# Performance work log

Hardware: AMD Instinct MI355X
Metric: run time of the kernel (lower is better)

Reference implementation:

```python
import jax, jax.numpy as jnp
import numpy as np

B, T, D, SPAN = 4, 4096, 1024, 128


def _windowed_attention(q, k, v, span):
    # Causal sliding-window attention: position t attends to [max(0, t-span+1), t].
    # Tiled as blocks of size span: each query block attends to its own block
    # plus the previous block (exactly covers the window), avoiding any [T,T]
    # or per-timestep materialization.
    B, T, D = q.shape
    S = span
    nb = T // S  # T chosen divisible by span
    qb = q.reshape(B, nb, S, D)
    kb = k.reshape(B, nb, S, D)
    vb = v.reshape(B, nb, S, D)
    pad = jnp.zeros((B, 1, S, D), dtype=q.dtype)
    kk = jnp.concatenate([jnp.concatenate([pad, kb[:, :-1]], axis=1), kb], axis=2)  # [B,nb,2S,D]
    vv = jnp.concatenate([jnp.concatenate([pad, vb[:, :-1]], axis=1), vb], axis=2)  # [B,nb,2S,D]
    scale = 1.0 / jnp.sqrt(jnp.asarray(D, dtype=q.dtype))
    scores = jnp.einsum('bnqd,bnkd->bnqk', qb, kk) * scale  # [B,nb,S,2S]
    n_idx = jnp.arange(nb)[:, None, None]      # block index
    q_idx = jnp.arange(S)[None, :, None]       # query offset within block
    k_idx = jnp.arange(2 * S)[None, None, :]   # key offset in [prev|cur] pair
    rel = k_idx - S - q_idx                    # key_pos - query_pos
    # window: -span+1 <= rel <= 0; first block's "previous" half is padding -> mask it
    mask = (rel <= 0) & (rel > -S) & ((n_idx > 0) | (k_idx >= S))
    neg = jnp.asarray(jnp.finfo(scores.dtype).min, dtype=scores.dtype)
    scores = jnp.where(mask, scores, neg)
    w = jax.nn.softmax(scores, axis=-1)
    out = jnp.einsum('bnqk,bnkd->bnqd', w, vv)
    return out.reshape(B, T, D)


def setup_inputs() -> dict:
    key = jax.random.key(0)
    ks = jax.random.split(key, 7)
    s = 1.0 / np.sqrt(D)
    return {
        'x': jax.random.normal(ks[0], (B, T, D), dtype=jnp.float32),
        'Wq': jax.random.normal(ks[1], (D, D), dtype=jnp.float32) * s,
        'bq': jax.random.normal(ks[2], (D,), dtype=jnp.float32) * s,
        'Wk': jax.random.normal(ks[3], (D, D), dtype=jnp.float32) * s,
        'bk': jax.random.normal(ks[4], (D,), dtype=jnp.float32) * s,
        'Wv': jax.random.normal(ks[5], (D, D), dtype=jnp.float32) * s,
        'bv': jax.random.normal(ks[6], (D,), dtype=jnp.float32) * s,
        'span': SPAN,
    }


def reference(x, Wq, bq, Wk, bk, Wv, bv, span):
    # torch nn.Linear: y = x @ W.T + b
    q = jnp.einsum('btd,ed->bte', x, Wq) + bq
    k = jnp.einsum('btd,ed->bte', x, Wk) + bk
    v = jnp.einsum('btd,ed->bte', x, Wv) + bv
    return _windowed_attention(q, k, v, span)
```

## Files before the change

kernel.cpp:

```cpp
#include <hip/hip_runtime.h>
#include <hip/hip_bf16.h>

#define BB 4
#define TT 4096
#define DD 1024
#define SS 128
#define MM (BB*TT)

typedef __attribute__((ext_vector_type(8))) short bf16x8;
typedef __attribute__((ext_vector_type(4))) short s16x4;
typedef __attribute__((ext_vector_type(4))) float f32x4;

#define VMCNT(N) asm volatile("s_waitcnt vmcnt(" #N ")" ::: "memory")
#define LGKM0()  asm volatile("s_waitcnt lgkmcnt(0)" ::: "memory")

__device__ __forceinline__ void block_sync() {
    asm volatile("" ::: "memory");
    __builtin_amdgcn_s_barrier();
    asm volatile("" ::: "memory");
}

__device__ __forceinline__ short f2bf(float f) {
    union { float f; unsigned u; } cv; cv.f = f;
    unsigned u = cv.u;
    u += 0x7fffu + ((u >> 16) & 1u);
    return (short)(u >> 16);
}

__device__ __forceinline__ void gload16(const short* g, short* l) {
    __builtin_amdgcn_global_load_lds(
        (const __attribute__((address_space(1))) void*)g,
        (__attribute__((address_space(3))) void*)l, 16, 0, 0);
}

__global__ __launch_bounds__(256) void cast_f32_bf16(
    const float* __restrict__ src, short* __restrict__ dst)
{
    const int i = (blockIdx.x * 256 + threadIdx.x) * 4;
    const float4 v = *(const float4*)(src + i);
    s16x4 o;
    o.x = f2bf(v.x); o.y = f2bf(v.y); o.z = f2bf(v.z); o.w = f2bf(v.w);
    *(s16x4*)(dst + i) = o;
}

__global__ __launch_bounds__(256) void cast_w3(
    const float* __restrict__ a, const float* __restrict__ b,
    const float* __restrict__ c, short* __restrict__ dst)
{
    const float* src = (blockIdx.y == 0) ? a : (blockIdx.y == 1) ? b : c;
    short* d = dst + (size_t)blockIdx.y * DD * DD;
    const int i = (blockIdx.x * 256 + threadIdx.x) * 4;
    const float4 v = *(const float4*)(src + i);
    s16x4 o;
    o.x = f2bf(v.x); o.y = f2bf(v.y); o.z = f2bf(v.z); o.w = f2bf(v.w);
    *(s16x4*)(d + i) = o;
}


#define MF(a_, b_, c_) ((GRP == 2)                                            \
    ? __builtin_amdgcn_mfma_f32_16x16x32_bf16((b_), (a_), (c_), 0, 0, 0)      \
    : __builtin_amdgcn_mfma_f32_16x16x32_bf16((a_), (b_), (c_), 0, 0, 0))

#define QKV_PHASE(ABASE, P, STAGE_STMT, VM_STMT)                              \
  do {                                                                        \
    bf16x8 af0k0 = *(const bf16x8*)((ABASE) + (((P)*2)*16   + c16) * 64 + sw0);\
    bf16x8 af0k1 = *(const bf16x8*)((ABASE) + (((P)*2)*16   + c16) * 64 + sw1);\
    bf16x8 af1k0 = *(const bf16x8*)((ABASE) + (((P)*2+1)*16 + c16) * 64 + sw0);\
    bf16x8 af1k1 = *(const bf16x8*)((ABASE) + (((P)*2+1)*16 + c16) * 64 + sw1);\
    STAGE_STMT;                                                               \
    block_sync();                                                             \
    LGKM0();                                                                  \
    __builtin_amdgcn_s_setprio(1);                                            \
    _Pragma("unroll")                                                         \
    for (int nj = 0; nj < 4; nj++) {                                          \
      acc[(P)*2][nj]   = MF(af0k0, bf[nj][0], acc[(P)*2][nj]);                \
      acc[(P)*2][nj]   = MF(af0k1, bf[nj][1], acc[(P)*2][nj]);                \
      acc[(P)*2+1][nj] = MF(af1k0, bf[nj][0], acc[(P)*2+1][nj]);              \
      acc[(P)*2+1][nj] = MF(af1k1, bf[nj][1], acc[(P)*2+1][nj]);              \
    }                                                                         \
    __builtin_amdgcn_s_setprio(0);                                            \
    VM_STMT;                                                                  \
    block_sync();                                                             \
  } while (0)

template<int GRP>
__device__ __forceinline__ void qkv_core(
    const short* __restrict__ X, const short* __restrict__ W,
    const float* __restrict__ bias,
    short* __restrict__ Y, short* __restrict__ vT,
    short* lds, const int m_base, const int n_base)
{
    const int tid  = threadIdx.x;
    const int wv   = tid >> 6, lane = tid & 63;
    const int wm   = wv >> 2,  wn   = wv & 3;
    const int quad = lane >> 4, c16 = lane & 15;
    const int swz  = c16 & 7;
    const int sw0  = ((quad)     ^ swz) * 8;
    const int sw1  = ((quad + 4) ^ swz) * 8;

    auto stageA = [&](int k0, int d, int h) {
        short* dst = lds + d * 16384 + h * 8192;
#pragma unroll
        for (int g = 0; g < 2; g++) {
            const int idx = g * 512 + tid;
            const int row = idx >> 3, slot = idx & 7;
            gload16(X + (size_t)(m_base + h * 128 + row) * DD + k0
                      + ((slot ^ (row & 7)) * 8),
                    dst + row * 64 + slot * 8);
        }
    };
    auto stageB = [&](int k0, int d, int h) {
        short* dst = lds + 32768 + d * 16384 + h * 8192;
#pragma unroll
        for (int g = 0; g < 2; g++) {
            const int idx = g * 512 + tid;
            const int row = idx >> 3, slot = idx & 7;
            gload16(W + (size_t)(n_base + h * 128 + row) * DD + k0
                      + ((slot ^ (row & 7)) * 8),
                    dst + row * 64 + slot * 8);
        }
    };

    f32x4 acc[8][4];
#pragma unroll
    for (int i = 0; i < 8; i++)
#pragma unroll
        for (int j = 0; j < 4; j++) acc[i][j] = (f32x4){0.f, 0.f, 0.f, 0.f};

    stageA(0, 0, 0);  stageA(0, 0, 1);
    stageB(0, 0, 0);  stageB(0, 0, 1);
    stageB(64, 1, 0); stageB(64, 1, 1);
    VMCNT(4);
    block_sync();

    const short* Abuf0 = lds + wm * 8192;
    const short* Abuf1 = lds + 16384 + wm * 8192;
    const short* Bbuf0 = lds + 32768 + (wn >> 1) * 8192 + (wn & 1) * 4096;
    const short* Bbuf1 = lds + 49152 + (wn >> 1) * 8192 + (wn & 1) * 4096;

    bf16x8 bf[4][2];

    for (int it = 0; it < 8; ++it) {
        const int k1 = it * 128 + 64;
        const int k2 = it * 128 + 128;
        const int k3 = it * 128 + 192;
        const bool more = (it < 7);

#pragma unroll
        for (int nj = 0; nj < 4; nj++) {
            bf[nj][0] = *(const bf16x8*)(Bbuf0 + (nj * 16 + c16) * 64 + sw0);
            bf[nj][1] = *(const bf16x8*)(Bbuf0 + (nj * 16 + c16) * 64 + sw1);
        }
        QKV_PHASE(Abuf0, 0, stageA(k1, 1, 0), ((void)0));
        QKV_PHASE(Abuf0, 1, stageA(k1, 1, 1), ((void)0));
        QKV_PHASE(Abuf0, 2, if (more) stageB(k2, 0, 0), ((void)0));
        QKV_PHASE(Abuf0, 3, if (more) stageB(k2, 0, 1),
                  if (more) { VMCNT(4); } else { VMCNT(0); });

#pragma unroll
        for (int nj = 0; nj < 4; nj++) {
            bf[nj][0] = *(const bf16x8*)(Bbuf1 + (nj * 16 + c16) * 64 + sw0);
            bf[nj][1] = *(const bf16x8*)(Bbuf1 + (nj * 16 + c16) * 64 + sw1);
        }
        QKV_PHASE(Abuf1, 0, if (more) stageA(k2, 0, 0), ((void)0));
        QKV_PHASE(Abuf1, 1, if (more) stageA(k2, 0, 1), ((void)0));
        QKV_PHASE(Abuf1, 2, if (more) stageB(k3, 1, 0), ((void)0));
        QKV_PHASE(Abuf1, 3, if (more) stageB(k3, 1, 1),
                  if (more) { VMCNT(4); } else { VMCNT(0); });
    }

    if (GRP != 2) {
#pragma unroll
        for (int nj = 0; nj < 4; nj++) {
            const int col = n_base + wn * 64 + nj * 16 + c16;
            const float bc = bias[col];
#pragma unroll
            for (int mi = 0; mi < 8; mi++) {
                const int row = m_base + wm * 128 + mi * 16 + quad * 4;
#pragma unroll
                for (int r = 0; r < 4; r++)
                    Y[(size_t)(row + r) * DD + col] = f2bf(acc[mi][nj][r] + bc);
            }
        }
    } else {
#pragma unroll
        for (int nj = 0; nj < 4; nj++) {
#pragma unroll
            for (int r = 0; r < 4; r++) {
                const int drow = n_base + wn * 64 + nj * 16 + quad * 4 + r;
                const float bc = bias[drow];
#pragma unroll
                for (int mi = 0; mi < 8; mi++) {
                    const int mcol = m_base + wm * 128 + mi * 16 + c16;
                    vT[((size_t)(mcol >> 12) * DD + drow) * TT + (mcol & 4095)]
                        = f2bf(acc[mi][nj][r] + bc);
                }
            }
        }
    }
}

__global__ __launch_bounds__(512, 2) void qkv_gemm8(
    const short* __restrict__ X, const short* __restrict__ W3,
    const float* __restrict__ bq, const float* __restrict__ bk,
    const float* __restrict__ bv,
    short* __restrict__ q, short* __restrict__ k, short* __restrict__ vT)
{
    __shared__ __align__(16) short lds[65536];
    const int bid = blockIdx.x;
    const int wg  = (bid & 7) * 96 + (bid >> 3);
    const int mt  = wg & 63;
    const int cn  = wg >> 6;
    const int grp = cn >> 2;
    const int nt  = cn & 3;
    const int m_base = mt * 256;
    const int n_base = nt * 256;
    if (grp == 0)      qkv_core<0>(X, W3,              bq, q, nullptr, lds, m_base, n_base);
    else if (grp == 1) qkv_core<1>(X, W3 + DD * DD,    bk, k, nullptr, lds, m_base, n_base);
    else               qkv_core<2>(X, W3 + 2 * DD * DD, bv, nullptr, vT, lds, m_base, n_base);
}

__global__ __launch_bounds__(512, 2) void attn_fused(
    const short* __restrict__ Q,
    const short* __restrict__ Kb,
    const short* __restrict__ VT,
    float* __restrict__ O)
{
    __shared__ short lds[78336];

    const int l   = blockIdx.x;
    const int xcd = l & 7;
    const int rr  = l >> 3;
    const int n   = xcd * 4 + (rr & 3);
    const int qh  = (rr >> 2) & 1;
    const int b   = rr >> 3;

    const int tid  = threadIdx.x;
    const int wv   = tid >> 6, lane = tid & 63;
    const int quad = lane >> 4, c16 = lane & 15;
    const int qt   = wv >> 1;
    const int kh   = wv & 1;
    const int dh   = wv & 1;

    const int qrow   = b * TT + n * SS + qh * 64;
    const int krow   = b * TT + n * SS - SS;
    const int bstart = b * TT;

    f32x4 acc[8];
#pragma unroll
    for (int j = 0; j < 8; j++) acc[j] = (f32x4){0.f, 0.f, 0.f, 0.f};

    auto stage1 = [&](int kk, int bi) {
        short* qb = lds + bi * 20480;
        short* kb = qb + 4096;
        const int k0 = kk * 64;
        {
            const int row = tid >> 3, slot = tid & 7;
            gload16(Q + (qrow + row) * DD + k0 + ((slot ^ (row & 7)) * 8),
                    qb + row * 64 + slot * 8);
        }
#pragma unroll
        for (int g = 0; g < 4; g++) {
            const int idx = g * 512 + tid;
            const int row = idx >> 3, slot = idx & 7;
            int grow = krow + row;
            if (grow < bstart) grow = bstart;
            gload16(Kb + grow * DD + k0 + ((slot ^ (row & 7)) * 8),
                    kb + row * 64 + slot * 8);
        }
    };

    const int sw7 = c16 & 7;

    stage1(0, 0);
    stage1(1, 1);
    for (int kk = 0; kk < 16; kk++) {
        if (kk < 15) { VMCNT(5); } else { VMCNT(0); }
        block_sync();
        if (kk < 14) stage1(kk + 2, (kk + 2) % 3);
        const short* qb = lds + (kk % 3) * 20480;
        const short* kb = qb + 4096;
        __builtin_amdgcn_s_setprio(1);
#pragma unroll
        for (int ks = 0; ks < 2; ks++) {
            const int slot = ((ks * 4 + quad) ^ sw7) * 8;
            bf16x8 a = *(const bf16x8*)(qb + (qt * 16 + c16) * 64 + slot);
#pragma unroll
            for (int j = 0; j < 8; j++) {
                bf16x8 bf = *(const bf16x8*)(kb + (kh * 128 + j * 16 + c16) * 64 + slot);
                acc[j] = __builtin_amdgcn_mfma_f32_16x16x32_bf16(a, bf, acc[j], 0, 0, 0);
            }
        }
        __builtin_amdgcn_s_setprio(0);
    }

    block_sync();

    const int tbase = n * SS - SS;
    auto stage2 = [&](int s, int bi) {
        short* vb = lds + bi * 16384;
        const int d0  = (s >> 1) * 128;
        const int khv = (s & 1) * 128;
#pragma unroll
        for (int g = 0; g < 4; g++) {
            const int idx = g * 512 + tid;
            const int row = idx >> 4, slot = idx & 15;
            int t = tbase + khv + ((slot ^ (row & 15)) * 8);
            if (t < 0) t = 0;
            gload16(VT + (size_t)(b * DD + d0 + row) * TT + t,
                    vb + row * 128 + slot * 8);
        }
    };
    stage2(0, 0);
    stage2(1, 1);

    short* Pb   = lds + 61440;
    float* smax = (float*)(lds + 49152);
    float* ssum = (float*)(lds + 49408);
    const float scale = 0.03125f;
    float mx4[4], sums[4];

#pragma unroll
    for (int r = 0; r < 4; r++) {
        const int q_idx = qh * 64 + qt * 16 + quad * 4 + r;
        float mx = -3.0e38f;
#pragma unroll
        for (int j = 0; j < 8; j++) {
            const int k_idx = kh * 128 + j * 16 + c16;
            const int rel = k_idx - SS - q_idx;
            const bool valid = (rel <= 0) & (rel > -SS) & ((n > 0) | (k_idx >= SS));
            const float sv = valid ? acc[j][r] * scale : -3.0e38f;
            acc[j][r] = sv;
            mx = fmaxf(mx, sv);
        }
#pragma unroll
        for (int o = 1; o < 16; o <<= 1) mx = fmaxf(mx, __shfl_xor(mx, o));
        mx4[r] = mx;
        if (c16 == 0) smax[(qt * 2 + kh) * 16 + quad * 4 + r] = mx;
    }
    LGKM0(); block_sync();

#pragma unroll
    for (int r = 0; r < 4; r++) {
        const float M = fmaxf(mx4[r], smax[(qt * 2 + (kh ^ 1)) * 16 + quad * 4 + r]);
        float sm = 0.f;
#pragma unroll
        for (int j = 0; j < 8; j++) {
            const float p = __expf(acc[j][r] - M);
            acc[j][r] = p;
            sm += p;
        }
#pragma unroll
        for (int o = 1; o < 16; o <<= 1) sm += __shfl_xor(sm, o);
        sums[r] = sm;
        if (c16 == 0) ssum[(qt * 2 + kh) * 16 + quad * 4 + r] = sm;
    }
    LGKM0(); block_sync();

#pragma unroll
    for (int r = 0; r < 4; r++) {
        const float inv = 1.0f / (sums[r] + ssum[(qt * 2 + (kh ^ 1)) * 16 + quad * 4 + r]);
#pragma unroll
        for (int j = 0; j < 8; j++)
            Pb[(qt * 16 + quad * 4 + r) * 264 + kh * 128 + j * 16 + c16] = f2bf(acc[j][r] * inv);
    }
    LGKM0();

    f32x4 o_all[32];
#pragma unroll
    for (int j = 0; j < 32; j++) o_all[j] = (f32x4){0.f, 0.f, 0.f, 0.f};

#pragma unroll
    for (int s = 0; s < 16; s++) {
        if (s < 15) { VMCNT(4); } else { VMCNT(0); }
        block_sync();
        if (s < 14) stage2(s + 2, (s + 2) % 3);
        const short* vb = lds + (s % 3) * 16384;
        const int khP = (s & 1) * 128;
        const int od  = (s >> 1) * 4;
        __builtin_amdgcn_s_setprio(1);
#pragma unroll
        for (int kc = 0; kc < 4; kc++) {
            bf16x8 a = *(const bf16x8*)(Pb + (qt * 16 + c16) * 264 + khP + kc * 32 + quad * 8);
#pragma unroll
            for (int jj = 0; jj < 4; jj++) {
                bf16x8 bvf = *(const bf16x8*)(vb + (dh * 64 + jj * 16 + c16) * 128
                                              + (((kc * 4 + quad) ^ c16) * 8));
                o_all[od + jj] = __builtin_amdgcn_mfma_f32_16x16x32_bf16(a, bvf, o_all[od + jj], 0, 0, 0);
            }
        }
        __builtin_amdgcn_s_setprio(0);
    }

#pragma unroll
    for (int d0i = 0; d0i < 8; d0i++)
#pragma unroll
        for (int jj = 0; jj < 4; jj++)
#pragma unroll
            for (int r = 0; r < 4; r++)
                O[(size_t)(qrow + qt * 16 + quad * 4 + r) * DD
                  + d0i * 128 + dh * 64 + jj * 16 + c16] = o_all[d0i * 4 + jj][r];
}

extern "C" void kernel_launch(void* const* d_in, const int* in_sizes, int n_in,
                              void* d_out, int out_size, void* d_ws, size_t ws_size,
                              hipStream_t stream) {
    const float* x  = (const float*)d_in[0];
    const float* Wq = (const float*)d_in[1];
    const float* bq = (const float*)d_in[2];
    const float* Wk = (const float*)d_in[3];
    const float* bk = (const float*)d_in[4];
    const float* Wv = (const float*)d_in[5];
    const float* bv = (const float*)d_in[6];
    float* out = (float*)d_out;

    char* ws = (char*)d_ws;
    const size_t SZ = (size_t)MM * DD * 2;
    short* q   = (short*)(ws);
    short* k   = (short*)(ws + SZ);
    short* vT  = (short*)(ws + 2 * SZ);
    short* xb  = (short*)(ws + 3 * SZ);
    short* w3b = (short*)(ws + 4 * SZ);

    dim3 blk(256);
    cast_f32_bf16<<<MM * DD / 1024, blk, 0, stream>>>(x, xb);
    cast_w3<<<dim3(DD * DD / 1024, 3), blk, 0, stream>>>(Wq, Wk, Wv, w3b);

    qkv_gemm8<<<768, 512, 0, stream>>>(xb, w3b, bq, bk, bv, q, k, vT);

    attn_fused<<<256, 512, 0, stream>>>(q, k, vT, out);
}
```

Before: 295.6 us.

## Trim attention key window to 192 keys per 64-query half and remap GEMM tiles

Each 64-query half-block of the attention kernel now loads and multiplies only the 192 keys its sliding window can reach, instead of the full 256-key previous-plus-current pair. This cuts the QK^T and PV MFMA work and the K/V loads by a quarter, and the V staging and output layout are reorganised into 256-wide d chunks over 12 stages. The QKV GEMM block-to-tile mapping is also changed so each XCD owns a contiguous set of M tiles, which should improve L2 reuse of X. The padding mask for the first block is recomputed with a per-half offset, and that offset has to stay correct.

```diff
diff --git a/kernel.cpp b/kernel.cpp
--- a/kernel.cpp
+++ b/kernel.cpp
@@ -208,9 +208,10 @@
 {
     __shared__ __align__(16) short lds[65536];
     const int bid = blockIdx.x;
-    const int wg  = (bid & 7) * 96 + (bid >> 3);
-    const int mt  = wg & 63;
-    const int cn  = wg >> 6;
+    const int x   = bid & 7;
+    const int j   = bid >> 3;
+    const int mt  = x * 8 + (j & 7);
+    const int cn  = j >> 3;
     const int grp = cn >> 2;
     const int nt  = cn & 3;
     const int m_base = mt * 256;
@@ -226,7 +227,7 @@
     const short* __restrict__ VT,
     float* __restrict__ O)
 {
-    __shared__ short lds[78336];
+    __shared__ short lds[74240];
 
     const int l   = blockIdx.x;
     const int xcd = l & 7;
@@ -243,15 +244,15 @@
     const int dh   = wv & 1;
 
     const int qrow   = b * TT + n * SS + qh * 64;
-    const int krow   = b * TT + n * SS - SS;
+    const int kbase  = b * TT + n * SS - SS + qh * 64;
     const int bstart = b * TT;
 
-    f32x4 acc[8];
-#pragma unroll
-    for (int j = 0; j < 8; j++) acc[j] = (f32x4){0.f, 0.f, 0.f, 0.f};
+    f32x4 acc[6];
+#pragma unroll
+    for (int j = 0; j < 6; j++) acc[j] = (f32x4){0.f, 0.f, 0.f, 0.f};
 
     auto stage1 = [&](int kk, int bi) {
-        short* qb = lds + bi * 20480;
+        short* qb = lds + bi * 16384;
         short* kb = qb + 4096;
         const int k0 = kk * 64;
         {
@@ -260,55 +261,55 @@
                     qb + row * 64 + slot * 8);
         }
 #pragma unroll
+        for (int g = 0; g < 3; g++) {
+            const int idx = g * 512 + tid;
+            const int row = idx >> 3, slot = idx & 7;
+            int grow = kbase + row;
+            if (grow < bstart) grow = bstart;
+            gload16(Kb + grow * DD + k0 + ((slot ^ (row & 7)) * 8),
+                    kb + row * 64 + slot * 8);
+        }
+    };
+
+    const int sw7 = c16 & 7;
+
+    stage1(0, 0);
+    stage1(1, 1);
+    for (int kk = 0; kk < 16; kk++) {
+        if (kk < 15) { VMCNT(4); } else { VMCNT(0); }
+        block_sync();
+        if (kk < 14) stage1(kk + 2, (kk + 2) % 3);
+        const short* qb = lds + (kk % 3) * 16384;
+        const short* kb = qb + 4096;
+        __builtin_amdgcn_s_setprio(1);
+#pragma unroll
+        for (int ks = 0; ks < 2; ks++) {
+            const int slot = ((ks * 4 + quad) ^ sw7) * 8;
+            bf16x8 a = *(const bf16x8*)(qb + (qt * 16 + c16) * 64 + slot);
+#pragma unroll
+            for (int j = 0; j < 6; j++) {
+                bf16x8 bf = *(const bf16x8*)(kb + (kh * 96 + j * 16 + c16) * 64 + slot);
+                acc[j] = __builtin_amdgcn_mfma_f32_16x16x32_bf16(a, bf, acc[j], 0, 0, 0);
+            }
+        }
+        __builtin_amdgcn_s_setprio(0);
+    }
+
+    block_sync();
+
+    const int tb2 = n * SS - SS + qh * 64;
+    auto stage2 = [&](int s, int bi) {
+        short* vb = lds + bi * 16384;
+        const int d0  = (s / 3) * 256;
+        const int kv0 = (s % 3) * 64;
+#pragma unroll
         for (int g = 0; g < 4; g++) {
             const int idx = g * 512 + tid;
             const int row = idx >> 3, slot = idx & 7;
-            int grow = krow + row;
-            if (grow < bstart) grow = bstart;
-            gload16(Kb + grow * DD + k0 + ((slot ^ (row & 7)) * 8),
-                    kb + row * 64 + slot * 8);
-        }
-    };
-
-    const int sw7 = c16 & 7;
-
-    stage1(0, 0);
-    stage1(1, 1);
-    for (int kk = 0; kk < 16; kk++) {
-        if (kk < 15) { VMCNT(5); } else { VMCNT(0); }
-        block_sync();
-        if (kk < 14) stage1(kk + 2, (kk + 2) % 3);
-        const short* qb = lds + (kk % 3) * 20480;
-        const short* kb = qb + 4096;
-        __builtin_amdgcn_s_setprio(1);
-#pragma unroll
-        for (int ks = 0; ks < 2; ks++) {
-            const int slot = ((ks * 4 + quad) ^ sw7) * 8;
-            bf16x8 a = *(const bf16x8*)(qb + (qt * 16 + c16) * 64 + slot);
-#pragma unroll
-            for (int j = 0; j < 8; j++) {
-                bf16x8 bf = *(const bf16x8*)(kb + (kh * 128 + j * 16 + c16) * 64 + slot);
-                acc[j] = __builtin_amdgcn_mfma_f32_16x16x32_bf16(a, bf, acc[j], 0, 0, 0);
-            }
-        }
-        __builtin_amdgcn_s_setprio(0);
-    }
-
-    block_sync();
-
-    const int tbase = n * SS - SS;
-    auto stage2 = [&](int s, int bi) {
-        short* vb = lds + bi * 16384;
-        const int d0  = (s >> 1) * 128;
-        const int khv = (s & 1) * 128;
-#pragma unroll
-        for (int g = 0; g < 4; g++) {
-            const int idx = g * 512 + tid;
-            const int row = idx >> 4, slot = idx & 15;
-            int t = tbase + khv + ((slot ^ (row & 15)) * 8);
+            int t = tb2 + kv0 + ((slot ^ (row & 7)) * 8);
             if (t < 0) t = 0;
             gload16(VT + (size_t)(b * DD + d0 + row) * TT + t,
-                    vb + row * 128 + slot * 8);
+                    vb + row * 64 + slot * 8);
         }
     };
     stage2(0, 0);
@@ -318,17 +319,18 @@
     float* smax = (float*)(lds + 49152);
     float* ssum = (float*)(lds + 49408);
     const float scale = 0.03125f;
+    const int   padk  = (n > 0) ? 0 : (SS - qh * 64);
     float mx4[4], sums[4];
 
 #pragma unroll
     for (int r = 0; r < 4; r++) {
-        const int q_idx = qh * 64 + qt * 16 + quad * 4 + r;
+        const int ql = qt * 16 + quad * 4 + r;
         float mx = -3.0e38f;
 #pragma unroll
-        for (int j = 0; j < 8; j++) {
-            const int k_idx = kh * 128 + j * 16 + c16;
-            const int rel = k_idx - SS - q_idx;
-            const bool valid = (rel <= 0) & (rel > -SS) & ((n > 0) | (k_idx >= SS));
+        for (int j = 0; j < 6; j++) {
+            const int k_local = kh * 96 + j * 16 + c16;
+            const int rel = k_local - SS - ql;
+            const bool valid = (rel <= 0) & (rel > -SS) & (k_local >= padk);
             const float sv = valid ? acc[j][r] * scale : -3.0e38f;
             acc[j][r] = sv;
             mx = fmaxf(mx, sv);
@@ -345,7 +347,7 @@
         const float M = fmaxf(mx4[r], smax[(qt * 2 + (kh ^ 1)) * 16 + quad * 4 + r]);
         float sm = 0.f;
 #pragma unroll
-        for (int j = 0; j < 8; j++) {
+        for (int j = 0; j < 6; j++) {
             const float p = __expf(acc[j][r] - M);
             acc[j][r] = p;
             sm += p;
@@ -361,8 +363,8 @@
     for (int r = 0; r < 4; r++) {
         const float inv = 1.0f / (sums[r] + ssum[(qt * 2 + (kh ^ 1)) * 16 + quad * 4 + r]);
 #pragma unroll
-        for (int j = 0; j < 8; j++)
-            Pb[(qt * 16 + quad * 4 + r) * 264 + kh * 128 + j * 16 + c16] = f2bf(acc[j][r] * inv);
+        for (int j = 0; j < 6; j++)
+            Pb[(qt * 16 + quad * 4 + r) * 200 + kh * 96 + j * 16 + c16] = f2bf(acc[j][r] * inv);
     }
     LGKM0();
 
@@ -371,21 +373,21 @@
     for (int j = 0; j < 32; j++) o_all[j] = (f32x4){0.f, 0.f, 0.f, 0.f};
 
 #pragma unroll
-    for (int s = 0; s < 16; s++) {
-        if (s < 15) { VMCNT(4); } else { VMCNT(0); }
+    for (int s = 0; s < 12; s++) {
+        if (s < 11) { VMCNT(4); } else { VMCNT(0); }
         block_sync();
-        if (s < 14) stage2(s + 2, (s + 2) % 3);
+        if (s < 10) stage2(s + 2, (s + 2) % 3);
         const short* vb = lds + (s % 3) * 16384;
-        const int khP = (s & 1) * 128;
-        const int od  = (s >> 1) * 4;
+        const int kv0 = (s % 3) * 64;
+        const int od  = (s / 3) * 8;
         __builtin_amdgcn_s_setprio(1);
 #pragma unroll
-        for (int kc = 0; kc < 4; kc++) {
-            bf16x8 a = *(const bf16x8*)(Pb + (qt * 16 + c16) * 264 + khP + kc * 32 + quad * 8);
-#pragma unroll
-            for (int jj = 0; jj < 4; jj++) {
-                bf16x8 bvf = *(const bf16x8*)(vb + (dh * 64 + jj * 16 + c16) * 128
-                                              + (((kc * 4 + quad) ^ c16) * 8));
+        for (int kc = 0; kc < 2; kc++) {
+            bf16x8 a = *(const bf16x8*)(Pb + (qt * 16 + c16) * 200 + kv0 + kc * 32 + quad * 8);
+#pragma unroll
+            for (int jj = 0; jj < 8; jj++) {
+                bf16x8 bvf = *(const bf16x8*)(vb + (dh * 128 + jj * 16 + c16) * 64
+                                              + (((kc * 4 + quad) ^ sw7) * 8));
                 o_all[od + jj] = __builtin_amdgcn_mfma_f32_16x16x32_bf16(a, bvf, o_all[od + jj], 0, 0, 0);
             }
         }
@@ -393,13 +395,13 @@
     }
 
 #pragma unroll
-    for (int d0i = 0; d0i < 8; d0i++)
-#pragma unroll
-        for (int jj = 0; jj < 4; jj++)
+    for (int g8 = 0; g8 < 4; g8++)
+#pragma unroll
+        for (int jj = 0; jj < 8; jj++)
 #pragma unroll
             for (int r = 0; r < 4; r++)
                 O[(size_t)(qrow + qt * 16 + quad * 4 + r) * DD
-                  + d0i * 128 + dh * 64 + jj * 16 + c16] = o_all[d0i * 4 + jj][r];
+                  + g8 * 256 + dh * 128 + jj * 16 + c16] = o_all[g8 * 8 + jj][r];
 }
 
 extern "C" void kernel_launch(void* const* d_in, const int* in_sizes, int n_in,
```

Result: faster. 272.3 us (-7.9%).
